# Kernel optimization log

Measured on AMD Instinct MI355X. Metric: run time of the kernel, lower is better.

## Reference

```python
import jax, jax.numpy as jnp
import numpy as np

B, T, D, H = 2, 2048, 1024, 16
HD = D // H  # 64


def _rotary_tables(t, hd):
    # standard RoPE cos/sin tables, shape [T, hd]
    inv_freq = 1.0 / (10000.0 ** (jnp.arange(0, hd, 2, dtype=jnp.float32) / hd))
    freqs = jnp.arange(t, dtype=jnp.float32)[:, None] * inv_freq[None, :]  # [T, hd/2]
    emb = jnp.concatenate([freqs, freqs], axis=-1)  # [T, hd]
    return jnp.cos(emb), jnp.sin(emb)


def setup_inputs() -> dict:
    key = jax.random.key(0)
    kx, kq, kk, kv, kp = jax.random.split(key, 5)
    x = jax.random.normal(kx, (B, T, D), dtype=jnp.float32)
    cos_t, sin_t = _rotary_tables(T, HD)
    cos = jnp.broadcast_to(cos_t[None], (B, T, HD)).astype(jnp.float32)
    sin = jnp.broadcast_to(sin_t[None], (B, T, HD)).astype(jnp.float32)
    scale = 0.02
    Wq = jax.random.normal(kq, (D, D), dtype=jnp.float32) * scale
    Wk = jax.random.normal(kk, (D, D), dtype=jnp.float32) * scale
    Wv = jax.random.normal(kv, (D, D), dtype=jnp.float32) * scale
    Wp = jax.random.normal(kp, (D, D), dtype=jnp.float32) * scale
    return {"x": x, "cos": cos, "sin": sin, "Wq": Wq, "Wk": Wk, "Wv": Wv, "Wp": Wp}


def _rotate_half(x):
    x1, x2 = jnp.split(x, 2, axis=-1)
    return jnp.concatenate([-x2, x1], axis=-1)


def reference(x, cos, sin, Wq, Wk, Wv, Wp):
    b, t, d = x.shape
    h, hd = H, HD
    # torch Linear: y = x @ W.T
    q = jnp.einsum('btd,ed->bte', x, Wq).reshape(b, t, h, hd)
    k = jnp.einsum('btd,ed->bte', x, Wk).reshape(b, t, h, hd)
    v = jnp.einsum('btd,ed->bte', x, Wv).reshape(b, t, h, hd)
    # RoPE, cos/sin [B,T,hd] -> broadcast over heads (unsqueeze_dim=2)
    c = cos[:, :, None, :]
    s = sin[:, :, None, :]
    q = q * c + _rotate_half(q) * s
    k = k * c + _rotate_half(k) * s
    # causal attention, softmax scale = 1/sqrt(head_dim) (flash_attn default)
    scale = 1.0 / np.sqrt(hd).astype(np.float32)
    scores = jnp.einsum('bqhd,bkhd->bhqk', q, k) * scale  # [B,H,T,T]
    mask = jnp.tril(jnp.ones((t, t), dtype=bool))
    scores = jnp.where(mask[None, None], scores, jnp.finfo(scores.dtype).min)
    probs = jax.nn.softmax(scores, axis=-1)
    out = jnp.einsum('bhqk,bkhd->bqhd', probs, v).reshape(b, t, d)
    return jnp.einsum('btd,ed->bte', out, Wp)
```

## Files before the change

### kernel.cpp

```cpp
#include <hip/hip_runtime.h>
#include <hip/hip_bf16.h>

typedef __attribute__((ext_vector_type(8))) short bf16x8s;
typedef __attribute__((ext_vector_type(4))) float f32x4;
typedef __attribute__((ext_vector_type(16))) float f32x16;
typedef __attribute__((ext_vector_type(4))) __bf16 bf16x4;
typedef __attribute__((ext_vector_type(8))) __bf16 bf16x8;

typedef const __attribute__((address_space(1))) void gvoid_t;
typedef __attribute__((address_space(3))) void lvoid_t;

constexpr int Bc = 2, Tc = 2048, Dc = 1024, Hc = 16, HDc = 64;
constexpr int Mc = Bc * Tc;

__global__ void cvt_all(const float* __restrict__ x,
                        const float* __restrict__ wq, const float* __restrict__ wk,
                        const float* __restrict__ wv, const float* __restrict__ wp,
                        __bf16* __restrict__ xb, __bf16* __restrict__ wb) {
  const int bid = blockIdx.x;
  const float* src;
  __bf16* dst;
  int i;
  if (bid < 4096) {
    src = x; dst = xb; i = (bid * 256 + threadIdx.x) * 4;
  } else {
    const int r = bid - 4096;
    const int w = r >> 10;
    src = (w == 0) ? wq : (w == 1) ? wk : (w == 2) ? wv : wp;
    dst = wb + (size_t)w * (Dc * Dc);
    i = ((r & 1023) * 256 + threadIdx.x) * 4;
  }
  float4 v = *(const float4*)(src + i);
  bf16x4 o;
  o[0] = (__bf16)v.x; o[1] = (__bf16)v.y; o[2] = (__bf16)v.z; o[3] = (__bf16)v.w;
  *(bf16x4*)(dst + i) = o;
}

__launch_bounds__(256, 2)
__global__ void gemm_qkv(const __bf16* __restrict__ A,
                         const __bf16* __restrict__ W,
                         __bf16* __restrict__ outb,
                         __bf16* __restrict__ vtout,
                         const float* __restrict__ cbt,
                         const float* __restrict__ sbt) {
  __shared__ __bf16 smem[2][128 * 64];
  __bf16* Alds = smem[0];
  __bf16* Blds = smem[1];
  const int tid = threadIdx.x;
  const int lane = tid & 63, wid = tid >> 6;
  const int wr = wid >> 1, wc = wid & 1;
  const int lr = lane & 15, lg = lane >> 4;
  const int lid = blockIdx.x + (int)gridDim.x * blockIdx.y;
  const int xcd = lid & 7, g = lid >> 3;
  const int brow = (xcd * 4 + (g & 3)) * 128;
  const int bcol = (g >> 2) * 128;
  const __bf16* Wm = W + (size_t)blockIdx.z * (Dc * Dc);

  f32x4 acc[4][4] = {};

  const char* Ag = (const char*)(A + (size_t)brow * Dc);
  const char* Bg = (const char*)(Wm + (size_t)bcol * Dc);
  const int r0 = tid >> 3;
  const int cb = (tid & 7) * 16;

  for (int k0 = 0; k0 < Dc; k0 += 64) {
#pragma unroll
    for (int i = 0; i < 4; ++i) {
      const int r = i * 32 + r0;
      const int ldsoff = (i * 256 + wid * 64) * 16;
      __builtin_amdgcn_global_load_lds(
          (gvoid_t*)(Ag + (size_t)r * (Dc * 2) + k0 * 2 + cb),
          (lvoid_t*)((char*)Alds + ldsoff), 16, 0, 0);
      __builtin_amdgcn_global_load_lds(
          (gvoid_t*)(Bg + (size_t)r * (Dc * 2) + k0 * 2 + cb),
          (lvoid_t*)((char*)Blds + ldsoff), 16, 0, 0);
    }
    __syncthreads();
#pragma unroll
    for (int kk = 0; kk < 2; ++kk) {
      const int col = kk * 32 + lg * 8;
      bf16x8s af[4], bfv[4];
#pragma unroll
      for (int m = 0; m < 4; ++m)
        af[m] = *(const bf16x8s*)(Alds + (wr * 64 + m * 16 + lr) * 64 + col);
#pragma unroll
      for (int n = 0; n < 4; ++n)
        bfv[n] = *(const bf16x8s*)(Blds + (wc * 64 + n * 16 + lr) * 64 + col);
#pragma unroll
      for (int m = 0; m < 4; ++m)
#pragma unroll
        for (int n = 0; n < 4; ++n)
          acc[m][n] = __builtin_amdgcn_mfma_f32_16x16x32_bf16(af[m], bfv[n], acc[m][n], 0, 0, 0);
    }
    __syncthreads();
  }

  const int z = blockIdx.z;
  if (z == 2) {
    const int bb = brow >> 11, t0b = brow & (Tc - 1);
    __bf16* tile_t = smem[0];
#pragma unroll
    for (int h2 = 0; h2 < 2; ++h2) {
      __syncthreads();
      if (wc == h2) {
#pragma unroll
        for (int n = 0; n < 4; ++n) {
#pragma unroll
          for (int m = 0; m < 4; ++m) {
            bf16x4 pb;
#pragma unroll
            for (int j = 0; j < 4; ++j) pb[j] = (__bf16)acc[m][n][j];
            *(bf16x4*)(tile_t + (n * 16 + lr) * 136 + wr * 64 + m * 16 + lg * 4) = pb;
          }
        }
      }
      __syncthreads();
#pragma unroll
      for (int pass = 0; pass < 4; ++pass) {
        const int r = pass * 16 + (tid >> 4);
        const int c8 = (tid & 15) * 8;
        bf16x8 vvv = *(const bf16x8*)(tile_t + r * 136 + c8);
        const int gn = bcol + h2 * 64 + r;
        const int h = gn >> 6, hd = gn & 63;
        *(bf16x8*)(vtout + (((size_t)bb * Hc + h) * HDc + hd) * Tc + t0b + c8) = vvv;
      }
    }
    return;
  }

  {
    const float scl = (z == 0) ? 0.18033688011112042f : 1.0f;
#pragma unroll
    for (int m = 0; m < 4; ++m) {
#pragma unroll
      for (int j = 0; j < 4; ++j) {
        const int gm = brow + wr * 64 + m * 16 + lg * 4 + j;
        const float* cbase = cbt + (size_t)gm * HDc;
        const float* sbase = sbt + (size_t)gm * HDc;
#pragma unroll
        for (int n = 0; n < 2; ++n) {
          const int i = n * 16 + lr;
          const float c0 = cbase[i], s0 = sbase[i];
          const float c1 = cbase[i + 32], s1 = sbase[i + 32];
          const float v0 = acc[m][n][j], v1 = acc[m][n + 2][j];
          acc[m][n][j]     = (v0 * c0 - v1 * s0) * scl;
          acc[m][n + 2][j] = (v1 * c1 + v0 * s1) * scl;
        }
      }
    }
    __bf16* dst = outb + (size_t)z * ((size_t)Mc * Dc);
#pragma unroll
    for (int m = 0; m < 4; ++m) {
#pragma unroll
      for (int j = 0; j < 4; ++j) {
        const int gm = brow + wr * 64 + m * 16 + lg * 4 + j;
        const int bb = gm >> 11, t = gm & (Tc - 1);
#pragma unroll
        for (int n = 0; n < 4; ++n) {
          const int gn = bcol + wc * 64 + n * 16 + lr;
          const int h = gn >> 6, hd = gn & 63;
          dst[(((size_t)bb * Hc + h) * Tc + t) * HDc + hd] = (__bf16)acc[m][n][j];
        }
      }
    }
  }
}

__launch_bounds__(256, 2)
__global__ void gemm_proj(const __bf16* __restrict__ A, const __bf16* __restrict__ W,
                          float* __restrict__ outf) {
  __shared__ __bf16 Alds[128 * 64];
  __shared__ __bf16 Blds[64 * 64];
  const int tid = threadIdx.x;
  const int lane = tid & 63, wid = tid >> 6;
  const int lr = lane & 15, lg = lane >> 4;
  const int lid = blockIdx.x + (int)gridDim.x * blockIdx.y;
  const int xcd = lid & 7, g = lid >> 3;
  const int brow = (xcd * 4 + (g & 3)) * 128;
  const int bcol = (g >> 2) * 64;
  f32x4 acc[2][4] = {};
  const char* Ag = (const char*)(A + (size_t)brow * Dc);
  const char* Bg = (const char*)(W + (size_t)bcol * Dc);
  const int r0 = tid >> 3;
  const int cb = (tid & 7) * 16;
  for (int k0 = 0; k0 < Dc; k0 += 64) {
#pragma unroll
    for (int i = 0; i < 4; ++i) {
      const int r = i * 32 + r0;
      const int ldsoff = (i * 256 + wid * 64) * 16;
      __builtin_amdgcn_global_load_lds(
          (gvoid_t*)(Ag + (size_t)r * (Dc * 2) + k0 * 2 + cb),
          (lvoid_t*)((char*)Alds + ldsoff), 16, 0, 0);
    }
#pragma unroll
    for (int i = 0; i < 2; ++i) {
      const int r = i * 32 + r0;
      const int ldsoff = (i * 256 + wid * 64) * 16;
      __builtin_amdgcn_global_load_lds(
          (gvoid_t*)(Bg + (size_t)r * (Dc * 2) + k0 * 2 + cb),
          (lvoid_t*)((char*)Blds + ldsoff), 16, 0, 0);
    }
    __syncthreads();
#pragma unroll
    for (int kk = 0; kk < 2; ++kk) {
      const int col = kk * 32 + lg * 8;
      bf16x8s af[2], bfv[4];
#pragma unroll
      for (int m = 0; m < 2; ++m)
        af[m] = *(const bf16x8s*)(Alds + (wid * 32 + m * 16 + lr) * 64 + col);
#pragma unroll
      for (int n = 0; n < 4; ++n)
        bfv[n] = *(const bf16x8s*)(Blds + (n * 16 + lr) * 64 + col);
#pragma unroll
      for (int m = 0; m < 2; ++m)
#pragma unroll
        for (int n = 0; n < 4; ++n)
          acc[m][n] = __builtin_amdgcn_mfma_f32_16x16x32_bf16(af[m], bfv[n], acc[m][n], 0, 0, 0);
    }
    __syncthreads();
  }
#pragma unroll
  for (int m = 0; m < 2; ++m)
#pragma unroll
    for (int j = 0; j < 4; ++j) {
      const int gm = brow + wid * 32 + m * 16 + lg * 4 + j;
#pragma unroll
      for (int n = 0; n < 4; ++n) {
        const int gn = bcol + n * 16 + lr;
        outf[(size_t)gm * Dc + gn] = acc[m][n][j];
      }
    }
}

__launch_bounds__(256, 2)
__global__ void attn_kernel(const __bf16* __restrict__ Q, const __bf16* __restrict__ K,
                            const __bf16* __restrict__ Vt, __bf16* __restrict__ O) {
  __shared__ __bf16 Klds[2][64 * 64];
  __shared__ __bf16 Vlds[2][64 * 64];
  const int f = blockIdx.x;
  const int xcd = f & 7, g = f >> 3;
  const int pass = g >> 4, g4 = g & 15;
  const int bh = xcd * 4 + pass;
  const int qt = ((pass ^ (pass >> 1)) & 1) ? (15 - g4) : g4;
  const int tid = threadIdx.x;
  const int lane = tid & 63, wid = tid >> 6;
  const int q31 = lane & 31, hh = lane >> 5;
  const int k3 = q31 & 7;
  const __bf16* Qp = Q + (size_t)bh * Tc * HDc;
  const char* Kb = (const char*)(K + (size_t)bh * Tc * HDc);
  const char* Vb = (const char*)(Vt + (size_t)bh * HDc * Tc);

  const int units = 2 * qt + 2;
  const int u_diag = 2 * qt + (wid >> 1);

  const int sr8 = wid * 8 + (lane >> 3);
  const int sxor = ((lane & 7) ^ ((lane >> 3) & 7)) << 4;
  const char* vsrc = Vb + (size_t)sr8 * (Tc * 2) + sxor;

  const int q0w = qt * 128 + wid * 32;
  bf16x8s qf[4];
#pragma unroll
  for (int ks = 0; ks < 4; ++ks)
    qf[ks] = *(const bf16x8s*)(Qp + (q0w + q31) * HDc + ks * 16 + hh * 8);

  const int b = bh >> 4, h = bh & 15;

  f32x16 acc0 = {}, acc1 = {};
  float lsum = 0.f;

#define STAGE(IT, BUF)                                                                   \
  do {                                                                                   \
    _Pragma("unroll")                                                                    \
    for (int i_ = 0; i_ < 2; ++i_) {                                                     \
      __builtin_amdgcn_global_load_lds(                                                  \
          (gvoid_t*)(Kb + (size_t)((IT) * 64 + i_ * 32 + sr8) * 128 + sxor),             \
          (lvoid_t*)((char*)Klds[BUF] + i_ * 4096 + wid * 1024), 16, 0, 0);              \
      __builtin_amdgcn_global_load_lds(                                                  \
          (gvoid_t*)(vsrc + (size_t)i_ * 32 * (Tc * 2) + (IT) * 128),                    \
          (lvoid_t*)((char*)Vlds[BUF] + i_ * 4096 + wid * 1024), 16, 0, 0);              \
    }                                                                                    \
  } while (0)

  STAGE(0, 0);
  asm volatile("s_waitcnt vmcnt(0)" ::: "memory");
  __builtin_amdgcn_sched_barrier(0);
  __builtin_amdgcn_s_barrier();
  __builtin_amdgcn_sched_barrier(0);

  for (int u = 0; u < units; ++u) {
    if (u + 1 < units) STAGE(u + 1, (u + 1) & 1);
    __builtin_amdgcn_sched_barrier(0);

    if (u <= u_diag) {
      const int kv0 = u * 64;
      const char* Kl = (const char*)Klds[u & 1];
      const char* Vl = (const char*)Vlds[u & 1];
      const bool fin = (u == u_diag);
      const int thr = q0w + q31 - kv0 - 4 * hh;

      unsigned w0[8], w1[8];
#pragma unroll
      for (int ct = 0; ct < 2; ++ct) {
        bf16x8s kf[4];
#pragma unroll
        for (int ks = 0; ks < 4; ++ks)
          kf[ks] = *(const bf16x8s*)(Kl + (ct * 32 + q31) * 128 + (((2 * ks + hh) ^ k3) << 4));
        f32x16 z = {};
        __builtin_amdgcn_s_setprio(1);
#pragma unroll
        for (int ks = 0; ks < 4; ++ks)
          z = __builtin_amdgcn_mfma_f32_32x32x16_bf16(kf[ks], qf[ks], z, 0, 0, 0);
        __builtin_amdgcn_s_setprio(0);
#pragma unroll
        for (int qd = 0; qd < 4; ++qd) {
          float e[4];
#pragma unroll
          for (int j = 0; j < 4; ++j) {
            float ev = __builtin_amdgcn_exp2f(z[qd * 4 + j]);
            if (fin && (ct * 32 + qd * 8 + j > thr)) ev = 0.f;
            lsum += ev;
            e[j] = ev;
          }
          const int n = ct * 4 + qd;
          asm("v_cvt_pk_bf16_f32 %0, %1, %2" : "=v"(w0[n]) : "v"(e[0]), "v"(e[1]));
          asm("v_cvt_pk_bf16_f32 %0, %1, %2" : "=v"(w1[n]) : "v"(e[2]), "v"(e[3]));
        }
      }

      bf16x8s pfr[4];
#pragma unroll
      for (int ks = 0; ks < 4; ++ks) {
        unsigned a = w0[2 * ks], bb2 = w0[2 * ks + 1];
        unsigned c = w1[2 * ks], d = w1[2 * ks + 1];
        asm volatile("v_permlane32_swap_b32 %0, %1" : "+v"(a), "+v"(bb2));
        asm volatile("v_permlane32_swap_b32 %0, %1" : "+v"(c), "+v"(d));
        union { unsigned u[4]; bf16x8s v; } uu;
        uu.u[0] = a; uu.u[1] = c; uu.u[2] = bb2; uu.u[3] = d;
        pfr[ks] = uu.v;
      }

      __builtin_amdgcn_s_setprio(1);
#pragma unroll
      for (int ks = 0; ks < 4; ++ks) {
        const int so = ((2 * ks + hh) ^ k3) << 4;
        const bf16x8s va0 = *(const bf16x8s*)(Vl + q31 * 128 + so);
        const bf16x8s va1 = *(const bf16x8s*)(Vl + (32 + q31) * 128 + so);
        acc0 = __builtin_amdgcn_mfma_f32_32x32x16_bf16(va0, pfr[ks], acc0, 0, 0, 0);
        acc1 = __builtin_amdgcn_mfma_f32_32x32x16_bf16(va1, pfr[ks], acc1, 0, 0, 0);
      }
      __builtin_amdgcn_s_setprio(0);
    }

    if (u + 1 < units) {
      asm volatile("s_waitcnt vmcnt(0)" ::: "memory");
      __builtin_amdgcn_sched_barrier(0);
      __builtin_amdgcn_s_barrier();
      __builtin_amdgcn_sched_barrier(0);
    }
  }
#undef STAGE

  const float lt = lsum + __shfl_xor(lsum, 32);
  const float linv = 1.f / lt;
  const int t = q0w + q31;
  __bf16* dst = O + ((size_t)b * Tc + t) * Dc + h * HDc;
#pragma unroll
  for (int qd = 0; qd < 4; ++qd) {
    bf16x4 o0, o1;
#pragma unroll
    for (int j = 0; j < 4; ++j) {
      o0[j] = (__bf16)(acc0[qd * 4 + j] * linv);
      o1[j] = (__bf16)(acc1[qd * 4 + j] * linv);
    }
    *(bf16x4*)(dst + qd * 8 + hh * 4) = o0;
    *(bf16x4*)(dst + 32 + qd * 8 + hh * 4) = o1;
  }
}

extern "C" void kernel_launch(void* const* d_in, const int* in_sizes, int n_in,
                              void* d_out, int out_size, void* d_ws, size_t ws_size,
                              hipStream_t stream) {
  const float* x   = (const float*)d_in[0];
  const float* cbt = (const float*)d_in[1];
  const float* sbt = (const float*)d_in[2];
  const float* Wq  = (const float*)d_in[3];
  const float* Wk  = (const float*)d_in[4];
  const float* Wv  = (const float*)d_in[5];
  const float* Wp  = (const float*)d_in[6];
  float* out = (float*)d_out;
  char* ws = (char*)d_ws;
  __bf16* xb = (__bf16*)(ws);
  __bf16* wb = (__bf16*)(ws + (8u << 20));
  __bf16* qb = (__bf16*)(ws + (16u << 20));
  __bf16* vt = (__bf16*)(ws + (40u << 20));
  __bf16* ao = (__bf16*)(ws + (48u << 20));
  __bf16* kb = qb + (size_t)Mc * Dc;

  cvt_all<<<8192, 256, 0, stream>>>(x, Wq, Wk, Wv, Wp, xb, wb);
  gemm_qkv<<<dim3(8, 32, 3), 256, 0, stream>>>(xb, wb, qb, vt, cbt, sbt);
  attn_kernel<<<512, 256, 0, stream>>>(qb, kb, vt, ao);
  gemm_proj<<<dim3(16, 32), 256, 0, stream>>>(ao, wb + 3u * (Dc * Dc), out);
}
```

Before: 115.5 us.

## Split attention KV tiles across wave pairs with 64-row query tiles and LDS reduction

Attention blocks now cover 64 query rows instead of 128, which doubles the grid to 1024 blocks. Within a block, two wave pairs share the same query rows and each takes half of every 64-key tile. Their partial accumulators and row sums are then combined through LDS at the end. The aim is more parallelism and occupancy (launch bounds raised to 4 blocks per CU) plus finer causal load balance, at the cost of an extra LDS reduction, reloading the K/V tiles for twice as many blocks, and tighter register limits.

```diff
diff --git a/kernel.cpp b/kernel.cpp
--- a/kernel.cpp
+++ b/kernel.cpp
@@ -232,32 +232,32 @@
     }
 }
 
-__launch_bounds__(256, 2)
+__launch_bounds__(256, 4)
 __global__ void attn_kernel(const __bf16* __restrict__ Q, const __bf16* __restrict__ K,
                             const __bf16* __restrict__ Vt, __bf16* __restrict__ O) {
   __shared__ __bf16 Klds[2][64 * 64];
   __shared__ __bf16 Vlds[2][64 * 64];
   const int f = blockIdx.x;
   const int xcd = f & 7, g = f >> 3;
-  const int pass = g >> 4, g4 = g & 15;
+  const int pass = g >> 5, g5 = g & 31;
   const int bh = xcd * 4 + pass;
-  const int qt = ((pass ^ (pass >> 1)) & 1) ? (15 - g4) : g4;
+  const int qt = (pass & 1) ? (31 - g5) : g5;
   const int tid = threadIdx.x;
   const int lane = tid & 63, wid = tid >> 6;
+  const int qh = wid >> 1, kp = wid & 1;
   const int q31 = lane & 31, hh = lane >> 5;
   const int k3 = q31 & 7;
   const __bf16* Qp = Q + (size_t)bh * Tc * HDc;
   const char* Kb = (const char*)(K + (size_t)bh * Tc * HDc);
   const char* Vb = (const char*)(Vt + (size_t)bh * HDc * Tc);
 
-  const int units = 2 * qt + 2;
-  const int u_diag = 2 * qt + (wid >> 1);
+  const int units = qt + 1;
 
   const int sr8 = wid * 8 + (lane >> 3);
   const int sxor = ((lane & 7) ^ ((lane >> 3) & 7)) << 4;
   const char* vsrc = Vb + (size_t)sr8 * (Tc * 2) + sxor;
 
-  const int q0w = qt * 128 + wid * 32;
+  const int q0w = qt * 64 + qh * 32;
   bf16x8s qf[4];
 #pragma unroll
   for (int ks = 0; ks < 4; ++ks)
@@ -291,62 +291,59 @@
     if (u + 1 < units) STAGE(u + 1, (u + 1) & 1);
     __builtin_amdgcn_sched_barrier(0);
 
-    if (u <= u_diag) {
-      const int kv0 = u * 64;
+    const bool last = (u == qt);
+    if (!last || qh == 1 || kp == 0) {
       const char* Kl = (const char*)Klds[u & 1];
       const char* Vl = (const char*)Vlds[u & 1];
-      const bool fin = (u == u_diag);
-      const int thr = q0w + q31 - kv0 - 4 * hh;
-
-      unsigned w0[8], w1[8];
-#pragma unroll
-      for (int ct = 0; ct < 2; ++ct) {
-        bf16x8s kf[4];
-#pragma unroll
-        for (int ks = 0; ks < 4; ++ks)
-          kf[ks] = *(const bf16x8s*)(Kl + (ct * 32 + q31) * 128 + (((2 * ks + hh) ^ k3) << 4));
-        f32x16 z = {};
-        __builtin_amdgcn_s_setprio(1);
-#pragma unroll
-        for (int ks = 0; ks < 4; ++ks)
-          z = __builtin_amdgcn_mfma_f32_32x32x16_bf16(kf[ks], qf[ks], z, 0, 0, 0);
-        __builtin_amdgcn_s_setprio(0);
-#pragma unroll
-        for (int qd = 0; qd < 4; ++qd) {
-          float e[4];
-#pragma unroll
-          for (int j = 0; j < 4; ++j) {
-            float ev = __builtin_amdgcn_exp2f(z[qd * 4 + j]);
-            if (fin && (ct * 32 + qd * 8 + j > thr)) ev = 0.f;
-            lsum += ev;
-            e[j] = ev;
-          }
-          const int n = ct * 4 + qd;
-          asm("v_cvt_pk_bf16_f32 %0, %1, %2" : "=v"(w0[n]) : "v"(e[0]), "v"(e[1]));
-          asm("v_cvt_pk_bf16_f32 %0, %1, %2" : "=v"(w1[n]) : "v"(e[2]), "v"(e[3]));
+      const bool fin = last && (qh == kp);
+      const int thr = q0w + q31 - u * 64 - kp * 32 - 4 * hh;
+
+      bf16x8s kf[4];
+#pragma unroll
+      for (int ks = 0; ks < 4; ++ks)
+        kf[ks] = *(const bf16x8s*)(Kl + (kp * 32 + q31) * 128 + (((2 * ks + hh) ^ k3) << 4));
+      f32x16 z = {};
+      __builtin_amdgcn_s_setprio(1);
+#pragma unroll
+      for (int ks = 0; ks < 4; ++ks)
+        z = __builtin_amdgcn_mfma_f32_32x32x16_bf16(kf[ks], qf[ks], z, 0, 0, 0);
+      __builtin_amdgcn_s_setprio(0);
+
+      unsigned w0[4], w1[4];
+#pragma unroll
+      for (int n = 0; n < 4; ++n) {
+        float e[4];
+#pragma unroll
+        for (int j = 0; j < 4; ++j) {
+          float ev = __builtin_amdgcn_exp2f(z[n * 4 + j]);
+          if (fin && (n * 8 + j > thr)) ev = 0.f;
+          lsum += ev;
+          e[j] = ev;
         }
-      }
-
-      bf16x8s pfr[4];
-#pragma unroll
-      for (int ks = 0; ks < 4; ++ks) {
-        unsigned a = w0[2 * ks], bb2 = w0[2 * ks + 1];
-        unsigned c = w1[2 * ks], d = w1[2 * ks + 1];
+        asm("v_cvt_pk_bf16_f32 %0, %1, %2" : "=v"(w0[n]) : "v"(e[0]), "v"(e[1]));
+        asm("v_cvt_pk_bf16_f32 %0, %1, %2" : "=v"(w1[n]) : "v"(e[2]), "v"(e[3]));
+      }
+
+      bf16x8s pfr[2];
+#pragma unroll
+      for (int ks2 = 0; ks2 < 2; ++ks2) {
+        unsigned a = w0[2 * ks2], bb2 = w0[2 * ks2 + 1];
+        unsigned c = w1[2 * ks2], d = w1[2 * ks2 + 1];
         asm volatile("v_permlane32_swap_b32 %0, %1" : "+v"(a), "+v"(bb2));
         asm volatile("v_permlane32_swap_b32 %0, %1" : "+v"(c), "+v"(d));
         union { unsigned u[4]; bf16x8s v; } uu;
         uu.u[0] = a; uu.u[1] = c; uu.u[2] = bb2; uu.u[3] = d;
-        pfr[ks] = uu.v;
+        pfr[ks2] = uu.v;
       }
 
       __builtin_amdgcn_s_setprio(1);
 #pragma unroll
-      for (int ks = 0; ks < 4; ++ks) {
-        const int so = ((2 * ks + hh) ^ k3) << 4;
+      for (int ks2 = 0; ks2 < 2; ++ks2) {
+        const int so = ((kp * 4 + 2 * ks2 + hh) ^ k3) << 4;
         const bf16x8s va0 = *(const bf16x8s*)(Vl + q31 * 128 + so);
         const bf16x8s va1 = *(const bf16x8s*)(Vl + (32 + q31) * 128 + so);
-        acc0 = __builtin_amdgcn_mfma_f32_32x32x16_bf16(va0, pfr[ks], acc0, 0, 0, 0);
-        acc1 = __builtin_amdgcn_mfma_f32_32x32x16_bf16(va1, pfr[ks], acc1, 0, 0, 0);
+        acc0 = __builtin_amdgcn_mfma_f32_32x32x16_bf16(va0, pfr[ks2], acc0, 0, 0, 0);
+        acc1 = __builtin_amdgcn_mfma_f32_32x32x16_bf16(va1, pfr[ks2], acc1, 0, 0, 0);
       }
       __builtin_amdgcn_s_setprio(0);
     }
@@ -360,20 +357,39 @@
   }
 #undef STAGE
 
-  const float lt = lsum + __shfl_xor(lsum, 32);
-  const float linv = 1.f / lt;
-  const int t = q0w + q31;
-  __bf16* dst = O + ((size_t)b * Tc + t) * Dc + h * HDc;
-#pragma unroll
-  for (int qd = 0; qd < 4; ++qd) {
-    bf16x4 o0, o1;
-#pragma unroll
-    for (int j = 0; j < 4; ++j) {
-      o0[j] = (__bf16)(acc0[qd * 4 + j] * linv);
-      o1[j] = (__bf16)(acc1[qd * 4 + j] * linv);
-    }
-    *(bf16x4*)(dst + qd * 8 + hh * 4) = o0;
-    *(bf16x4*)(dst + 32 + qd * 8 + hh * 4) = o1;
+  __syncthreads();
+  float* tp = (qh == 0) ? (float*)(&Klds[0][0]) : (float*)(&Vlds[0][0]);
+  if (kp == 1) {
+#pragma unroll
+    for (int i = 0; i < 16; ++i) {
+      tp[i * 64 + lane] = acc0[i];
+      tp[1024 + i * 64 + lane] = acc1[i];
+    }
+    tp[2048 + lane] = lsum;
+  }
+  __syncthreads();
+  if (kp == 0) {
+#pragma unroll
+    for (int i = 0; i < 16; ++i) {
+      acc0[i] += tp[i * 64 + lane];
+      acc1[i] += tp[1024 + i * 64 + lane];
+    }
+    lsum += tp[2048 + lane];
+    const float lt = lsum + __shfl_xor(lsum, 32);
+    const float linv = 1.f / lt;
+    const int t = q0w + q31;
+    __bf16* dst = O + ((size_t)b * Tc + t) * Dc + h * HDc;
+#pragma unroll
+    for (int qd = 0; qd < 4; ++qd) {
+      bf16x4 o0, o1;
+#pragma unroll
+      for (int j = 0; j < 4; ++j) {
+        o0[j] = (__bf16)(acc0[qd * 4 + j] * linv);
+        o1[j] = (__bf16)(acc1[qd * 4 + j] * linv);
+      }
+      *(bf16x4*)(dst + qd * 8 + hh * 4) = o0;
+      *(bf16x4*)(dst + 32 + qd * 8 + hh * 4) = o1;
+    }
   }
 }
 
@@ -398,6 +414,6 @@
 
   cvt_all<<<8192, 256, 0, stream>>>(x, Wq, Wk, Wv, Wp, xb, wb);
   gemm_qkv<<<dim3(8, 32, 3), 256, 0, stream>>>(xb, wb, qb, vt, cbt, sbt);
-  attn_kernel<<<512, 256, 0, stream>>>(qb, kb, vt, ao);
+  attn_kernel<<<1024, 256, 0, stream>>>(qb, kb, vt, ao);
   gemm_proj<<<dim3(16, 32), 256, 0, stream>>>(ao, wb + 3u * (Dc * Dc), out);
 }
```

Result: faster. 99.88 us (-13.6%).
